# Kernel tuning notes

Measured on AMD Instinct MI355X. Metric: run time of the kernel, lower is better.

## Reference

```python
import jax, jax.numpy as jnp
import numpy as np

N = 2048  # number of graph nodes


def setup_inputs() -> dict:
    key = jax.random.key(0)
    k1, k2, k3, k4 = jax.random.split(key, 4)
    # dense non-negative adjacency / association matrix
    A = jax.random.uniform(k1, (N, N), dtype=jnp.float32)
    # GTConv weights: layer0.conv1, layer0.conv2, layer1.conv1 (each (2,1,1,1))
    w1a = jax.random.normal(k2, (2, 1, 1, 1), dtype=jnp.float32)
    w1b = jax.random.normal(k3, (2, 1, 1, 1), dtype=jnp.float32)
    w2a = jax.random.normal(k4, (2, 1, 1, 1), dtype=jnp.float32)
    return {"A": A, "w1a": w1a, "w1b": w1b, "w2a": w2a}


def _gtconv(A4, w):
    # A4: (1,1,n,n); w: (2,1,1,1). softmax over dim=1 (singleton -> ones),
    # broadcast-multiply -> (2,1,n,n), sum over dim 0 -> (1,n,n)
    sw = jax.nn.softmax(w, axis=1)
    return jnp.sum(A4 * sw, axis=0)


def _norm(H):
    # H: (n,n). H <- diag(deg)^-1 @ (H + I), expressed as a row-scale
    # (identical math to the diagonal mm in the original).
    n = H.shape[0]
    H = H + jnp.eye(n, dtype=H.dtype)
    deg = jnp.sum(H, axis=1)
    deg = jnp.where(deg <= 1e-10, jnp.ones_like(deg), deg)
    return H / deg[:, None]


def reference(A, w1a, w1b, w2a):
    A4 = A[None, None]  # (1,1,n,n) after the forward's unsqueeze + broadcast
    # layer 0 (first=True)
    a = _gtconv(A4, w1a)            # (1,n,n)
    b = _gtconv(A4, w1b)            # (1,n,n)
    H = jnp.matmul(a, b)            # (1,n,n)
    # layer 1 (first=False): normalization of H[0], then bmm with conv(A)
    H_ = _norm(H[0])[None]          # (1,n,n)
    a2 = _gtconv(A4, w2a)           # (1,n,n)
    H2 = jnp.matmul(H_, a2)         # (1,n,n)
    return H2
```

## Files before the change

### kernel.cpp

```cpp
#include <hip/hip_runtime.h>
#include <stdint.h>

#define N 2048
#define TILE 128
#define BK 32
#define KHALF 1024
#define KI (KHALF / BK)
#define LDSW 40
#define ABUF 5120
#define NN ((size_t)N * (size_t)N)

typedef unsigned short u16;
typedef __bf16 bf16x8 __attribute__((ext_vector_type(8)));
typedef unsigned short ushortx8 __attribute__((ext_vector_type(8)));
typedef float floatx4 __attribute__((ext_vector_type(4)));

static __device__ __forceinline__ u16 f2bf(float f) {
  unsigned int u = __builtin_bit_cast(unsigned int, f);
  return (u16)((u + 0x7fffu + ((u >> 16) & 1u)) >> 16);
}

__global__ void cast_tr(const float* __restrict__ A, u16* __restrict__ Ab,
                        u16* __restrict__ Abt) {
  __shared__ float tile[32][33];
  const int tx = threadIdx.x, ty = threadIdx.y;
  const int c = blockIdx.x * 32 + tx;
#pragma unroll
  for (int i = 0; i < 4; i++) {
    const int r = blockIdx.y * 32 + ty + i * 8;
    const float v = A[r * N + c];
    Ab[r * N + c] = f2bf(v);
    tile[ty + i * 8][tx] = v;
  }
  __syncthreads();
  const int r2 = blockIdx.y * 32 + tx;
#pragma unroll
  for (int i = 0; i < 4; i++) {
    const int c2 = blockIdx.x * 32 + ty + i * 8;
    Abt[c2 * N + r2] = f2bf(tile[tx][ty + i * 8]);
  }
}

__device__ __forceinline__ void gemm_core(u16* smem, const u16* __restrict__ L,
                                          const u16* __restrict__ Rt,
                                          floatx4 acc[4][4]) {
  const int t = threadIdx.x;
  const int g = t >> 8;
  const int tl = t & 255;
  const int row0 = blockIdx.y * TILE;
  const int col0 = blockIdx.x * TILE;

  const int srow = tl >> 1;
  const int sc = (tl & 1) * 16;
  const u16* gA = L + (size_t)(row0 + srow) * N + g * KHALF + sc;
  const u16* gB = Rt + (size_t)(col0 + srow) * N + g * KHALF + sc;
  const int wbA = g * (2 * ABUF) + srow * LDSW + sc;
  const int wbB = 20480 + wbA;

  const int lane = t & 63;
  const int wg = (t >> 6) & 3;
  const int wr = (wg >> 1) * 64;
  const int wc = (wg & 1) * 64;
  const int lr = lane & 15;
  const int q = lane >> 4;
  const int raA = g * (2 * ABUF) + (wr + lr) * LDSW + q * 8;
  const int raB = 20480 + g * (2 * ABUF) + (wc + lr) * LDSW + q * 8;

#pragma unroll
  for (int i = 0; i < 4; i++)
#pragma unroll
    for (int j = 0; j < 4; j++) acc[i][j] = (floatx4){0.f, 0.f, 0.f, 0.f};

  ushortx8 rA[4][2], rB[4][2];
#pragma unroll
  for (int s = 0; s < 3; s++) {
    rA[s][0] = *(const ushortx8*)(gA + s * BK);
    rA[s][1] = *(const ushortx8*)(gA + s * BK + 8);
    rB[s][0] = *(const ushortx8*)(gB + s * BK);
    rB[s][1] = *(const ushortx8*)(gB + s * BK + 8);
  }
  *(ushortx8*)(&smem[wbA]) = rA[0][0];
  *(ushortx8*)(&smem[wbA + 8]) = rA[0][1];
  *(ushortx8*)(&smem[wbB]) = rB[0][0];
  *(ushortx8*)(&smem[wbB + 8]) = rB[0][1];

#define GSTEP(i, s)                                                           \
  {                                                                           \
    __syncthreads();                                                          \
    if ((i) + 3 < KI) {                                                       \
      rA[((s) + 3) & 3][0] = *(const ushortx8*)(gA + ((i) + 3) * BK);         \
      rA[((s) + 3) & 3][1] = *(const ushortx8*)(gA + ((i) + 3) * BK + 8);     \
      rB[((s) + 3) & 3][0] = *(const ushortx8*)(gB + ((i) + 3) * BK);         \
      rB[((s) + 3) & 3][1] = *(const ushortx8*)(gB + ((i) + 3) * BK + 8);     \
    }                                                                         \
    bf16x8 af[4], bq[4];                                                      \
    _Pragma("unroll") for (int mt = 0; mt < 4; mt++) af[mt] =                 \
        __builtin_bit_cast(bf16x8, *(const ushortx8*)&smem[                   \
            raA + ((s) & 1) * ABUF + mt * 16 * LDSW]);                        \
    _Pragma("unroll") for (int nt = 0; nt < 4; nt++) bq[nt] =                 \
        __builtin_bit_cast(bf16x8, *(const ushortx8*)&smem[                   \
            raB + ((s) & 1) * ABUF + nt * 16 * LDSW]);                        \
    _Pragma("unroll") for (int mt = 0; mt < 4; mt++)                          \
        _Pragma("unroll") for (int nt = 0; nt < 4; nt++) acc[mt][nt] =        \
            __builtin_amdgcn_mfma_f32_16x16x32_bf16(af[mt], bq[nt],           \
                                                    acc[mt][nt], 0, 0, 0);    \
    if ((i) + 1 < KI) {                                                       \
      const int nb = (((s) + 1) & 1) * ABUF;                                  \
      *(ushortx8*)(&smem[wbA + nb]) = rA[((s) + 1) & 3][0];                   \
      *(ushortx8*)(&smem[wbA + nb + 8]) = rA[((s) + 1) & 3][1];               \
      *(ushortx8*)(&smem[wbB + nb]) = rB[((s) + 1) & 3][0];                   \
      *(ushortx8*)(&smem[wbB + nb + 8]) = rB[((s) + 1) & 3][1];               \
    }                                                                         \
  }

  for (int io = 0; io < KI; io += 4) {
    GSTEP(io + 0, 0)
    GSTEP(io + 1, 1)
    GSTEP(io + 2, 2)
    GSTEP(io + 3, 3)
  }
#undef GSTEP
}

__device__ __forceinline__ void combine(u16* smem, floatx4 acc[4][4]) {
  float* smf = (float*)smem;
  const int t = threadIdx.x;
  const int g = t >> 8;
  const int lane = t & 63;
  const int wg = (t >> 6) & 3;
  __syncthreads();
  if (g == 1) {
#pragma unroll
    for (int mt = 0; mt < 4; mt++)
#pragma unroll
      for (int nt = 0; nt < 4; nt++)
        *(floatx4*)&smf[wg * 4096 + (mt * 4 + nt) * 256 + lane * 4] =
            acc[mt][nt];
  }
  __syncthreads();
  if (g == 0) {
#pragma unroll
    for (int mt = 0; mt < 4; mt++)
#pragma unroll
      for (int nt = 0; nt < 4; nt++)
        acc[mt][nt] += *(const floatx4*)&smf[wg * 4096 + (mt * 4 + nt) * 256 +
                                             lane * 4];
  }
}

__global__ __launch_bounds__(512, 2) void gemm1(const u16* __restrict__ Ab,
                                                const u16* __restrict__ Abt,
                                                u16* __restrict__ Mb,
                                                float* __restrict__ deg) {
  __shared__ __align__(16) u16 smem[40960];
  floatx4 acc[4][4];
  gemm_core(smem, Ab, Abt, acc);
  combine(smem, acc);

  float* rs = (float*)smem + 16384;
  const int t = threadIdx.x;
  const int row0 = blockIdx.y * TILE, col0 = blockIdx.x * TILE;
  if (t < TILE) rs[t] = 0.f;
  __syncthreads();
  if ((t >> 8) == 0) {
    const int lane = t & 63, wg = (t >> 6) & 3;
    const int wr = (wg >> 1) * 64, wc = (wg & 1) * 64;
    const int lr = lane & 15, q = lane >> 4;
    float trs[4][4];
#pragma unroll
    for (int mt = 0; mt < 4; mt++)
#pragma unroll
      for (int r = 0; r < 4; r++) trs[mt][r] = 0.f;
#pragma unroll
    for (int mt = 0; mt < 4; mt++)
#pragma unroll
      for (int nt = 0; nt < 4; nt++)
#pragma unroll
        for (int r = 0; r < 4; r++) {
          const float v = acc[mt][nt][r];
          const int rr = row0 + wr + mt * 16 + q * 4 + r;
          const int cc = col0 + wc + nt * 16 + lr;
          Mb[(size_t)rr * N + cc] = f2bf(v);
          trs[mt][r] += v;
        }
#pragma unroll
    for (int mt = 0; mt < 4; mt++)
#pragma unroll
      for (int r = 0; r < 4; r++)
        atomicAdd(&rs[wr + mt * 16 + q * 4 + r], trs[mt][r]);
  }
  __syncthreads();
  if (t < TILE) atomicAdd(&deg[row0 + t], rs[t]);
}

__global__ __launch_bounds__(512, 2) void gemm2(const u16* __restrict__ Mb,
                                                const u16* __restrict__ Abt,
                                                const float* __restrict__ A,
                                                const float* __restrict__ deg,
                                                float* __restrict__ out) {
  __shared__ __align__(16) u16 smem[40960];
  floatx4 acc[4][4];
  gemm_core(smem, Mb, Abt, acc);
  combine(smem, acc);

  const int t = threadIdx.x;
  if ((t >> 8) != 0) return;
  const int row0 = blockIdx.y * TILE, col0 = blockIdx.x * TILE;
  const int lane = t & 63, wg = (t >> 6) & 3;
  const int wr = (wg >> 1) * 64, wc = (wg & 1) * 64;
  const int lr = lane & 15, q = lane >> 4;
#pragma unroll
  for (int mt = 0; mt < 4; mt++)
#pragma unroll
    for (int r = 0; r < 4; r++) {
      const int rr = row0 + wr + mt * 16 + q * 4 + r;
      float d = 4.f * deg[rr] + 1.f;
      if (d <= 1e-10f) d = 1.f;
      const float rd = 1.f / d;
#pragma unroll
      for (int nt = 0; nt < 4; nt++) {
        const int cc = col0 + wc + nt * 16 + lr;
        out[(size_t)rr * N + cc] =
            (8.f * acc[mt][nt][r] + 2.f * A[(size_t)rr * N + cc]) * rd;
      }
    }
}

extern "C" void kernel_launch(void* const* d_in, const int* in_sizes, int n_in,
                              void* d_out, int out_size, void* d_ws, size_t ws_size,
                              hipStream_t stream) {
  const float* A = (const float*)d_in[0];
  float* out = (float*)d_out;
  char* ws = (char*)d_ws;
  u16* Ab = (u16*)ws;
  u16* Abt = (u16*)(ws + NN * 2);
  u16* Mb = (u16*)(ws + NN * 4);
  float* deg = (float*)(ws + NN * 6);

  hipMemsetAsync(deg, 0, N * sizeof(float), stream);
  cast_tr<<<dim3(N / 32, N / 32), dim3(32, 8), 0, stream>>>(A, Ab, Abt);
  gemm1<<<dim3(16, 16), 512, 0, stream>>>(Ab, Abt, Mb, deg);
  gemm2<<<dim3(16, 16), 512, 0, stream>>>(Mb, Abt, A, deg, out);
}
```

Before: 142.9 us.

## Replace split-K 128x128 tiles with 128x64 full-K tiles and drop LDS combine

```diff
diff --git a/kernel.cpp b/kernel.cpp
--- a/kernel.cpp
+++ b/kernel.cpp
@@ -2,12 +2,14 @@
 #include <stdint.h>
 
 #define N 2048
-#define TILE 128
+#define TM 128
+#define TN 64
 #define BK 32
-#define KHALF 1024
-#define KI (KHALF / BK)
+#define KI (N / BK)
 #define LDSW 40
 #define ABUF 5120
+#define BBUF 2560
+#define BOFF (2 * ABUF)
 #define NN ((size_t)N * (size_t)N)
 
 typedef unsigned short u16;
@@ -43,74 +45,72 @@
 
 __device__ __forceinline__ void gemm_core(u16* smem, const u16* __restrict__ L,
                                           const u16* __restrict__ Rt,
-                                          floatx4 acc[4][4]) {
+                                          floatx4 acc[4][2]) {
   const int t = threadIdx.x;
-  const int g = t >> 8;
-  const int tl = t & 255;
-  const int row0 = blockIdx.y * TILE;
-  const int col0 = blockIdx.x * TILE;
-
-  const int srow = tl >> 1;
-  const int sc = (tl & 1) * 16;
-  const u16* gA = L + (size_t)(row0 + srow) * N + g * KHALF + sc;
-  const u16* gB = Rt + (size_t)(col0 + srow) * N + g * KHALF + sc;
-  const int wbA = g * (2 * ABUF) + srow * LDSW + sc;
-  const int wbB = 20480 + wbA;
+  const int row0 = blockIdx.y * TM;
+  const int col0 = blockIdx.x * TN;
+
+  const int srA = t >> 1;
+  const int scA = (t & 1) * 16;
+  const u16* gA = L + (size_t)(row0 + srA) * N + scA;
+  const int wbA = srA * LDSW + scA;
+  const int srB = t >> 2;
+  const int scB = (t & 3) * 8;
+  const u16* gB = Rt + (size_t)(col0 + srB) * N + scB;
+  const int wbB = BOFF + srB * LDSW + scB;
 
   const int lane = t & 63;
-  const int wg = (t >> 6) & 3;
-  const int wr = (wg >> 1) * 64;
-  const int wc = (wg & 1) * 64;
+  const int w = t >> 6;
+  const int wr = (w >> 1) * 64;
+  const int wc = (w & 1) * 32;
   const int lr = lane & 15;
   const int q = lane >> 4;
-  const int raA = g * (2 * ABUF) + (wr + lr) * LDSW + q * 8;
-  const int raB = 20480 + g * (2 * ABUF) + (wc + lr) * LDSW + q * 8;
+  const int raA = (wr + lr) * LDSW + q * 8;
+  const int raB = BOFF + (wc + lr) * LDSW + q * 8;
 
 #pragma unroll
   for (int i = 0; i < 4; i++)
 #pragma unroll
-    for (int j = 0; j < 4; j++) acc[i][j] = (floatx4){0.f, 0.f, 0.f, 0.f};
-
-  ushortx8 rA[4][2], rB[4][2];
+    for (int j = 0; j < 2; j++) acc[i][j] = (floatx4){0.f, 0.f, 0.f, 0.f};
+
+  ushortx8 rA[4][2], rB[4];
 #pragma unroll
   for (int s = 0; s < 3; s++) {
     rA[s][0] = *(const ushortx8*)(gA + s * BK);
     rA[s][1] = *(const ushortx8*)(gA + s * BK + 8);
-    rB[s][0] = *(const ushortx8*)(gB + s * BK);
-    rB[s][1] = *(const ushortx8*)(gB + s * BK + 8);
+    rB[s] = *(const ushortx8*)(gB + s * BK);
   }
   *(ushortx8*)(&smem[wbA]) = rA[0][0];
   *(ushortx8*)(&smem[wbA + 8]) = rA[0][1];
-  *(ushortx8*)(&smem[wbB]) = rB[0][0];
-  *(ushortx8*)(&smem[wbB + 8]) = rB[0][1];
+  *(ushortx8*)(&smem[wbB]) = rB[0];
+  __syncthreads();
 
 #define GSTEP(i, s)                                                           \
   {                                                                           \
-    __syncthreads();                                                          \
     if ((i) + 3 < KI) {                                                       \
       rA[((s) + 3) & 3][0] = *(const ushortx8*)(gA + ((i) + 3) * BK);         \
       rA[((s) + 3) & 3][1] = *(const ushortx8*)(gA + ((i) + 3) * BK + 8);     \
-      rB[((s) + 3) & 3][0] = *(const ushortx8*)(gB + ((i) + 3) * BK);         \
-      rB[((s) + 3) & 3][1] = *(const ushortx8*)(gB + ((i) + 3) * BK + 8);     \
+      rB[((s) + 3) & 3] = *(const ushortx8*)(gB + ((i) + 3) * BK);            \
     }                                                                         \
-    bf16x8 af[4], bq[4];                                                      \
+    bf16x8 af[4], bq[2];                                                      \
     _Pragma("unroll") for (int mt = 0; mt < 4; mt++) af[mt] =                 \
         __builtin_bit_cast(bf16x8, *(const ushortx8*)&smem[                   \
             raA + ((s) & 1) * ABUF + mt * 16 * LDSW]);                        \
-    _Pragma("unroll") for (int nt = 0; nt < 4; nt++) bq[nt] =                 \
+    _Pragma("unroll") for (int nt = 0; nt < 2; nt++) bq[nt] =                 \
         __builtin_bit_cast(bf16x8, *(const ushortx8*)&smem[                   \
-            raB + ((s) & 1) * ABUF + nt * 16 * LDSW]);                        \
+            raB + ((s) & 1) * BBUF + nt * 16 * LDSW]);                        \
     _Pragma("unroll") for (int mt = 0; mt < 4; mt++)                          \
-        _Pragma("unroll") for (int nt = 0; nt < 4; nt++) acc[mt][nt] =        \
+        _Pragma("unroll") for (int nt = 0; nt < 2; nt++) acc[mt][nt] =        \
             __builtin_amdgcn_mfma_f32_16x16x32_bf16(af[mt], bq[nt],           \
                                                     acc[mt][nt], 0, 0, 0);    \
+    __syncthreads();   \
     if ((i) + 1 < KI) {                                                       \
-      const int nb = (((s) + 1) & 1) * ABUF;                                  \
-      *(ushortx8*)(&smem[wbA + nb]) = rA[((s) + 1) & 3][0];                   \
-      *(ushortx8*)(&smem[wbA + nb + 8]) = rA[((s) + 1) & 3][1];               \
-      *(ushortx8*)(&smem[wbB + nb]) = rB[((s) + 1) & 3][0];                   \
-      *(ushortx8*)(&smem[wbB + nb + 8]) = rB[((s) + 1) & 3][1];               \
+      *(ushortx8*)(&smem[wbA + (((s) + 1) & 1) * ABUF]) = rA[((s) + 1) & 3][0]; \
+      *(ushortx8*)(&smem[wbA + (((s) + 1) & 1) * ABUF + 8]) =                 \
+          rA[((s) + 1) & 3][1];                                               \
+      *(ushortx8*)(&smem[wbB + (((s) + 1) & 1) * BBUF]) = rB[((s) + 1) & 3];  \
     }                                                                         \
+    __syncthreads();                   \
   }
 
   for (int io = 0; io < KI; io += 4) {
@@ -122,92 +122,61 @@
 #undef GSTEP
 }
 
-__device__ __forceinline__ void combine(u16* smem, floatx4 acc[4][4]) {
-  float* smf = (float*)smem;
-  const int t = threadIdx.x;
-  const int g = t >> 8;
-  const int lane = t & 63;
-  const int wg = (t >> 6) & 3;
-  __syncthreads();
-  if (g == 1) {
-#pragma unroll
-    for (int mt = 0; mt < 4; mt++)
-#pragma unroll
-      for (int nt = 0; nt < 4; nt++)
-        *(floatx4*)&smf[wg * 4096 + (mt * 4 + nt) * 256 + lane * 4] =
-            acc[mt][nt];
-  }
-  __syncthreads();
-  if (g == 0) {
-#pragma unroll
-    for (int mt = 0; mt < 4; mt++)
-#pragma unroll
-      for (int nt = 0; nt < 4; nt++)
-        acc[mt][nt] += *(const floatx4*)&smf[wg * 4096 + (mt * 4 + nt) * 256 +
-                                             lane * 4];
-  }
-}
-
-__global__ __launch_bounds__(512, 2) void gemm1(const u16* __restrict__ Ab,
+__global__ __launch_bounds__(256, 2) void gemm1(const u16* __restrict__ Ab,
                                                 const u16* __restrict__ Abt,
                                                 u16* __restrict__ Mb,
                                                 float* __restrict__ deg) {
-  __shared__ __align__(16) u16 smem[40960];
-  floatx4 acc[4][4];
+  __shared__ __align__(16) u16 smem[2 * ABUF + 2 * BBUF];
+  floatx4 acc[4][2];
   gemm_core(smem, Ab, Abt, acc);
-  combine(smem, acc);
-
-  float* rs = (float*)smem + 16384;
+
+  float* rs = (float*)smem;
   const int t = threadIdx.x;
-  const int row0 = blockIdx.y * TILE, col0 = blockIdx.x * TILE;
-  if (t < TILE) rs[t] = 0.f;
-  __syncthreads();
-  if ((t >> 8) == 0) {
-    const int lane = t & 63, wg = (t >> 6) & 3;
-    const int wr = (wg >> 1) * 64, wc = (wg & 1) * 64;
-    const int lr = lane & 15, q = lane >> 4;
-    float trs[4][4];
-#pragma unroll
-    for (int mt = 0; mt < 4; mt++)
-#pragma unroll
-      for (int r = 0; r < 4; r++) trs[mt][r] = 0.f;
-#pragma unroll
-    for (int mt = 0; mt < 4; mt++)
-#pragma unroll
-      for (int nt = 0; nt < 4; nt++)
-#pragma unroll
-        for (int r = 0; r < 4; r++) {
-          const float v = acc[mt][nt][r];
-          const int rr = row0 + wr + mt * 16 + q * 4 + r;
-          const int cc = col0 + wc + nt * 16 + lr;
-          Mb[(size_t)rr * N + cc] = f2bf(v);
-          trs[mt][r] += v;
-        }
-#pragma unroll
-    for (int mt = 0; mt < 4; mt++)
-#pragma unroll
-      for (int r = 0; r < 4; r++)
-        atomicAdd(&rs[wr + mt * 16 + q * 4 + r], trs[mt][r]);
-  }
-  __syncthreads();
-  if (t < TILE) atomicAdd(&deg[row0 + t], rs[t]);
-}
-
-__global__ __launch_bounds__(512, 2) void gemm2(const u16* __restrict__ Mb,
+  const int row0 = blockIdx.y * TM, col0 = blockIdx.x * TN;
+  if (t < TM) rs[t] = 0.f;
+  __syncthreads();
+  const int lane = t & 63, w = t >> 6;
+  const int wr = (w >> 1) * 64, wc = (w & 1) * 32;
+  const int lr = lane & 15, q = lane >> 4;
+  float trs[4][4];
+#pragma unroll
+  for (int mt = 0; mt < 4; mt++)
+#pragma unroll
+    for (int r = 0; r < 4; r++) trs[mt][r] = 0.f;
+#pragma unroll
+  for (int mt = 0; mt < 4; mt++)
+#pragma unroll
+    for (int nt = 0; nt < 2; nt++)
+#pragma unroll
+      for (int r = 0; r < 4; r++) {
+        const float v = acc[mt][nt][r];
+        const int rr = row0 + wr + mt * 16 + q * 4 + r;
+        const int cc = col0 + wc + nt * 16 + lr;
+        Mb[(size_t)rr * N + cc] = f2bf(v);
+        trs[mt][r] += v;
+      }
+#pragma unroll
+  for (int mt = 0; mt < 4; mt++)
+#pragma unroll
+    for (int r = 0; r < 4; r++)
+      atomicAdd(&rs[wr + mt * 16 + q * 4 + r], trs[mt][r]);
+  __syncthreads();
+  if (t < TM) atomicAdd(&deg[row0 + t], rs[t]);
+}
+
+__global__ __launch_bounds__(256, 2) void gemm2(const u16* __restrict__ Mb,
                                                 const u16* __restrict__ Abt,
                                                 const float* __restrict__ A,
                                                 const float* __restrict__ deg,
                                                 float* __restrict__ out) {
-  __shared__ __align__(16) u16 smem[40960];
-  floatx4 acc[4][4];
+  __shared__ __align__(16) u16 smem[2 * ABUF + 2 * BBUF];
+  floatx4 acc[4][2];
   gemm_core(smem, Mb, Abt, acc);
-  combine(smem, acc);
 
   const int t = threadIdx.x;
-  if ((t >> 8) != 0) return;
-  const int row0 = blockIdx.y * TILE, col0 = blockIdx.x * TILE;
-  const int lane = t & 63, wg = (t >> 6) & 3;
-  const int wr = (wg >> 1) * 64, wc = (wg & 1) * 64;
+  const int row0 = blockIdx.y * TM, col0 = blockIdx.x * TN;
+  const int lane = t & 63, w = t >> 6;
+  const int wr = (w >> 1) * 64, wc = (w & 1) * 32;
   const int lr = lane & 15, q = lane >> 4;
 #pragma unroll
   for (int mt = 0; mt < 4; mt++)
@@ -218,7 +187,7 @@
       if (d <= 1e-10f) d = 1.f;
       const float rd = 1.f / d;
 #pragma unroll
-      for (int nt = 0; nt < 4; nt++) {
+      for (int nt = 0; nt < 2; nt++) {
         const int cc = col0 + wc + nt * 16 + lr;
         out[(size_t)rr * N + cc] =
             (8.f * acc[mt][nt][r] + 2.f * A[(size_t)rr * N + cc]) * rd;
@@ -239,6 +208,6 @@
 
   hipMemsetAsync(deg, 0, N * sizeof(float), stream);
   cast_tr<<<dim3(N / 32, N / 32), dim3(32, 8), 0, stream>>>(A, Ab, Abt);
-  gemm1<<<dim3(16, 16), 512, 0, stream>>>(Ab, Abt, Mb, deg);
-  gemm2<<<dim3(16, 16), 512, 0, stream>>>(Mb, Abt, A, deg, out);
-}
+  gemm1<<<dim3(N / TN, N / TM), 256, 0, stream>>>(Ab, Abt, Mb, deg);
+  gemm2<<<dim3(N / TN, N / TM), 256, 0, stream>>>(Mb, Abt, A, deg, out);
+}
```

Result: slower. 158.2 us (+10.7%).
